# Kernel tuning notes

Measured on AMD Instinct MI355X. Metric: run time of the kernel, lower is better.

Reference implementation:

```python
import jax, jax.numpy as jnp
import numpy as np

NUM_CLASSES = 21  # O + 10 entity types x {B, I}


def setup_inputs() -> dict:
    key = jax.random.key(0)
    k1, k2, k3, k4 = jax.random.split(key, 4)
    S_SENT, L, D = 256, 128, 768
    return {
        "support_emb": jax.random.normal(k1, (S_SENT, L, D), dtype=jnp.float32),
        "query_emb": jax.random.normal(k2, (S_SENT, L, D), dtype=jnp.float32),
        "support_label": jax.random.randint(k3, (S_SENT, L), 0, NUM_CLASSES, dtype=jnp.int32),
        "support_text_mask": jax.random.randint(k4, (S_SENT, L), 0, 2, dtype=jnp.int32),
    }


def reference(support_emb, query_emb, support_label, support_text_mask):
    D = support_emb.shape[-1]
    emb = support_emb.reshape(-1, D)                      # [Ns, D]
    lab = support_label.reshape(-1)                       # [Ns]
    msk = support_text_mask.reshape(-1).astype(emb.dtype) # [Ns]

    # __get_proto__: per-class mean over masked support tokens (segment-mean via one-hot GEMM)
    onehot = jax.nn.one_hot(lab, NUM_CLASSES, dtype=emb.dtype) * msk[:, None]  # [Ns, C]
    class_sum = jnp.einsum("nc,nd->cd", onehot, emb)      # [C, D]
    counts = onehot.sum(axis=0)                           # [C]
    proto = jnp.where(counts[:, None] > 0,
                      class_sum / jnp.maximum(counts, 1.0)[:, None],
                      0.0)                                 # absent classes -> zero vector

    # __batch_dist__: -||q - p||^2 expanded as GEMM (same math, no NxCxD tensor)
    Q = query_emb.reshape(-1, D)                          # [Nq, D] (query mask all-ones)
    logits = (2.0 * Q @ proto.T
              - jnp.sum(Q * Q, axis=-1, keepdims=True)
              - jnp.sum(proto * proto, axis=-1)[None, :])  # [Nq, C]

    pred = jnp.argmax(logits, axis=1)
    return logits, pred
```

## Files before the change

kernel.cpp:

```cpp
#include <hip/hip_runtime.h>

#define NS 32768
#define NQ 32768
#define DIM 768
#define NC 21

#define WS_CS    0
#define WS_CNT   16128
#define WS_PROTO 16384
#define WS_PNORM 32512
#define WS_ZERO_FLOATS 16384

__global__ __launch_bounds__(256) void k_counts(const int* __restrict__ lab,
                                                const int* __restrict__ msk,
                                                float* __restrict__ ws) {
    __shared__ int cnt[NC];
    int tid = threadIdx.x;
    if (tid < NC) cnt[tid] = 0;
    __syncthreads();
    int idx = blockIdx.x * 256 + tid;
    int stride = gridDim.x * 256;
    for (int i = idx; i < NS; i += stride) {
        if (msk[i]) atomicAdd(&cnt[lab[i]], 1);
    }
    __syncthreads();
    if (tid < NC && cnt[tid] > 0) atomicAdd(&ws[WS_CNT + tid], (float)cnt[tid]);
}

#define K1_TOK 256
#define K1_DCOLS 256
__global__ __launch_bounds__(256) void k_classsum(const float* __restrict__ emb,
                                                  const int* __restrict__ lab,
                                                  const int* __restrict__ msk,
                                                  float* __restrict__ ws) {
    __shared__ float acc[NC][K1_DCOLS];
    int tid = threadIdx.x;
    for (int i = tid; i < NC * K1_DCOLS; i += 256) ((float*)acc)[i] = 0.f;
    __syncthreads();

    int chunk = blockIdx.x;
    int dblk  = blockIdx.y;
    int dbase = dblk * K1_DCOLS;
    int t0    = chunk * K1_TOK;
    const float* ebase = emb + (size_t)t0 * DIM + dbase;

    #pragma unroll 1
    for (int tt = 0; tt < K1_TOK; tt += 4) {
        float v0 = ebase[(size_t)(tt + 0) * DIM + tid];
        float v1 = ebase[(size_t)(tt + 1) * DIM + tid];
        float v2 = ebase[(size_t)(tt + 2) * DIM + tid];
        float v3 = ebase[(size_t)(tt + 3) * DIM + tid];
        int t = t0 + tt;
        int c0 = lab[t + 0], m0 = msk[t + 0];
        int c1 = lab[t + 1], m1 = msk[t + 1];
        int c2 = lab[t + 2], m2 = msk[t + 2];
        int c3 = lab[t + 3], m3 = msk[t + 3];
        if (m0) acc[c0][tid] += v0;
        if (m1) acc[c1][tid] += v1;
        if (m2) acc[c2][tid] += v2;
        if (m3) acc[c3][tid] += v3;
    }
    __syncthreads();

    #pragma unroll
    for (int c = 0; c < NC; ++c) {
        atomicAdd(&ws[WS_CS + c * DIM + dbase + tid], acc[c][tid]);
    }
}

__global__ __launch_bounds__(256) void k_proto(float* __restrict__ ws) {
    int c = blockIdx.x;
    int tid = threadIdx.x;
    float cnt = ws[WS_CNT + c];
    float scale = (cnt > 0.f) ? (1.f / cnt) : 0.f;
    float ssq = 0.f;
    for (int d = tid; d < DIM; d += 256) {
        float p = ws[WS_CS + c * DIM + d] * scale;
        ws[WS_PROTO + c * DIM + d] = p;
        ssq += p * p;
    }
    #pragma unroll
    for (int m = 32; m; m >>= 1) ssq += __shfl_xor(ssq, m);
    __shared__ float w4[4];
    if ((tid & 63) == 0) w4[tid >> 6] = ssq;
    __syncthreads();
    if (tid == 0) ws[WS_PNORM + c] = w4[0] + w4[1] + w4[2] + w4[3];
}

__global__ __launch_bounds__(256) void k_logits(const float* __restrict__ qemb,
                                                const float* __restrict__ ws,
                                                float* __restrict__ out) {
    int wid  = threadIdx.x >> 6;
    int lane = threadIdx.x & 63;
    int q = blockIdx.x * 4 + wid;

    const float4* q4 = (const float4*)qemb + (size_t)q * (DIM / 4);
    float4 a = q4[lane], b = q4[lane + 64], c4 = q4[lane + 128];

    float qn = a.x * a.x + a.y * a.y + a.z * a.z + a.w * a.w
             + b.x * b.x + b.y * b.y + b.z * b.z + b.w * b.w
             + c4.x * c4.x + c4.y * c4.y + c4.z * c4.z + c4.w * c4.w;
    #pragma unroll
    for (int m = 32; m; m >>= 1) qn += __shfl_xor(qn, m);

    const float4* p4 = (const float4*)(ws + WS_PROTO);
    float logit[NC];
    #pragma unroll
    for (int c = 0; c < NC; ++c) {
        const float4* pr = p4 + c * (DIM / 4);
        float4 x = pr[lane], y = pr[lane + 64], z = pr[lane + 128];
        float d = a.x * x.x + a.y * x.y + a.z * x.z + a.w * x.w
                + b.x * y.x + b.y * y.y + b.z * y.z + b.w * y.w
                + c4.x * z.x + c4.y * z.y + c4.z * z.z + c4.w * z.w;
        #pragma unroll
        for (int m = 32; m; m >>= 1) d += __shfl_xor(d, m);
        logit[c] = 2.f * d - qn - ws[WS_PNORM + c];
    }

    float best = logit[0];
    int bi = 0;
    #pragma unroll
    for (int c = 1; c < NC; ++c) {
        if (logit[c] > best) { best = logit[c]; bi = c; }
    }

    float myv = 0.f;
    #pragma unroll
    for (int c = 0; c < NC; ++c) myv = (lane == c) ? logit[c] : myv;
    float* lrow = out + (size_t)q * NC;
    if (lane < NC) lrow[lane] = myv;
    if (lane == 0) out[(size_t)NQ * NC + q] = (float)bi;
}

extern "C" void kernel_launch(void* const* d_in, const int* in_sizes, int n_in,
                              void* d_out, int out_size, void* d_ws, size_t ws_size,
                              hipStream_t stream) {
    const float* semb = (const float*)d_in[0];
    const float* qemb = (const float*)d_in[1];
    const int*   lab  = (const int*)d_in[2];
    const int*   msk  = (const int*)d_in[3];
    float* ws  = (float*)d_ws;
    float* out = (float*)d_out;

    hipMemsetAsync(d_ws, 0, WS_ZERO_FLOATS * sizeof(float), stream);
    k_counts<<<64, 256, 0, stream>>>(lab, msk, ws);
    k_classsum<<<dim3(NS / K1_TOK, 3), 256, 0, stream>>>(semb, lab, msk, ws);
    k_proto<<<NC, 256, 0, stream>>>(ws);
    k_logits<<<NQ / 4, 256, 0, stream>>>(qemb, ws, out);
}
```

Measured before the change: 305.6 us.

## Fuse proto into logits, register-accumulate class sums, multi-row DPP reductions

Class sums are accumulated in per-thread registers using wave-uniform labels broadcast via readfirstlane and select-FMA, replacing shared-memory read-modify-write, with a one-step prefetch of embedding rows. The separate prototype kernel is removed; each logits block normalizes class sums into shared memory and computes prototype norms itself. The logits kernel processes four query rows per wave with DPP-based wave reductions and defers the query-norm subtraction until after the argmax. This trades redundant per-block prototype setup and more register pressure for fewer launches and less global/LDS traffic.

```diff
diff --git a/kernel.cpp b/kernel.cpp
--- a/kernel.cpp
+++ b/kernel.cpp
@@ -5,11 +5,24 @@
 #define DIM 768
 #define NC 21
 
-#define WS_CS    0
-#define WS_CNT   16128
-#define WS_PROTO 16384
-#define WS_PNORM 32512
-#define WS_ZERO_FLOATS 16384
+#define WS_CS   0
+#define WS_CNT  16128
+#define WS_ZERO 16149
+
+__device__ inline float wave_allsum(float x) {
+    x += __shfl_xor(x, 32);
+    x += __shfl_xor(x, 16);
+    int xi;
+    xi = __builtin_amdgcn_update_dpp(0, __float_as_int(x), 0x128, 0xF, 0xF, false);
+    x += __int_as_float(xi);
+    xi = __builtin_amdgcn_update_dpp(0, __float_as_int(x), 0x124, 0xF, 0xF, false);
+    x += __int_as_float(xi);
+    xi = __builtin_amdgcn_update_dpp(0, __float_as_int(x), 0x122, 0xF, 0xF, false);
+    x += __int_as_float(xi);
+    xi = __builtin_amdgcn_update_dpp(0, __float_as_int(x), 0x121, 0xF, 0xF, false);
+    x += __int_as_float(xi);
+    return x;
+}
 
 __global__ __launch_bounds__(256) void k_counts(const int* __restrict__ lab,
                                                 const int* __restrict__ msk,
@@ -27,109 +40,165 @@
     if (tid < NC && cnt[tid] > 0) atomicAdd(&ws[WS_CNT + tid], (float)cnt[tid]);
 }
 
-#define K1_TOK 256
-#define K1_DCOLS 256
-__global__ __launch_bounds__(256) void k_classsum(const float* __restrict__ emb,
+__global__ __launch_bounds__(768) void k_classsum(const float* __restrict__ emb,
                                                   const int* __restrict__ lab,
                                                   const int* __restrict__ msk,
                                                   float* __restrict__ ws) {
-    __shared__ float acc[NC][K1_DCOLS];
+    __shared__ int lmc[128];
     int tid = threadIdx.x;
-    for (int i = tid; i < NC * K1_DCOLS; i += 256) ((float*)acc)[i] = 0.f;
-    __syncthreads();
-
-    int chunk = blockIdx.x;
-    int dblk  = blockIdx.y;
-    int dbase = dblk * K1_DCOLS;
-    int t0    = chunk * K1_TOK;
-    const float* ebase = emb + (size_t)t0 * DIM + dbase;
-
-    #pragma unroll 1
-    for (int tt = 0; tt < K1_TOK; tt += 4) {
-        float v0 = ebase[(size_t)(tt + 0) * DIM + tid];
-        float v1 = ebase[(size_t)(tt + 1) * DIM + tid];
-        float v2 = ebase[(size_t)(tt + 2) * DIM + tid];
-        float v3 = ebase[(size_t)(tt + 3) * DIM + tid];
-        int t = t0 + tt;
-        int c0 = lab[t + 0], m0 = msk[t + 0];
-        int c1 = lab[t + 1], m1 = msk[t + 1];
-        int c2 = lab[t + 2], m2 = msk[t + 2];
-        int c3 = lab[t + 3], m3 = msk[t + 3];
-        if (m0) acc[c0][tid] += v0;
-        if (m1) acc[c1][tid] += v1;
-        if (m2) acc[c2][tid] += v2;
-        if (m3) acc[c3][tid] += v3;
-    }
-    __syncthreads();
-
-    #pragma unroll
+    int t0 = blockIdx.x * 128;
+    if (tid < 128) {
+        int i = t0 + tid;
+        lmc[tid] = msk[i] ? lab[i] : 255;
+    }
+    __syncthreads();
+
+    float acc[NC];
+#pragma unroll
+    for (int c = 0; c < NC; ++c) acc[c] = 0.f;
+
+    const float* ecol = emb + (size_t)t0 * DIM + tid;
+
+    auto process = [&](int tb, float v0, float v1, float v2, float v3) {
+        int cu0 = __builtin_amdgcn_readfirstlane(lmc[tb + 0]);
+        int cu1 = __builtin_amdgcn_readfirstlane(lmc[tb + 1]);
+        int cu2 = __builtin_amdgcn_readfirstlane(lmc[tb + 2]);
+        int cu3 = __builtin_amdgcn_readfirstlane(lmc[tb + 3]);
+#pragma unroll
+        for (int c = 0; c < NC; ++c) {
+            float s0 = (cu0 == c) ? 1.f : 0.f;
+            float s1 = (cu1 == c) ? 1.f : 0.f;
+            float s2 = (cu2 == c) ? 1.f : 0.f;
+            float s3 = (cu3 == c) ? 1.f : 0.f;
+            acc[c] = fmaf(s0, v0, acc[c]);
+            acc[c] = fmaf(s1, v1, acc[c]);
+            acc[c] = fmaf(s2, v2, acc[c]);
+            acc[c] = fmaf(s3, v3, acc[c]);
+        }
+    };
+
+    float v0 = ecol[(size_t)0 * DIM];
+    float v1 = ecol[(size_t)1 * DIM];
+    float v2 = ecol[(size_t)2 * DIM];
+    float v3 = ecol[(size_t)3 * DIM];
+    for (int g = 0; g < 31; ++g) {
+        int tb = g * 4;
+        float n0 = ecol[(size_t)(tb + 4) * DIM];
+        float n1 = ecol[(size_t)(tb + 5) * DIM];
+        float n2 = ecol[(size_t)(tb + 6) * DIM];
+        float n3 = ecol[(size_t)(tb + 7) * DIM];
+        process(tb, v0, v1, v2, v3);
+        v0 = n0; v1 = n1; v2 = n2; v3 = n3;
+    }
+    process(124, v0, v1, v2, v3);
+
+#pragma unroll
     for (int c = 0; c < NC; ++c) {
-        atomicAdd(&ws[WS_CS + c * DIM + dbase + tid], acc[c][tid]);
-    }
-}
-
-__global__ __launch_bounds__(256) void k_proto(float* __restrict__ ws) {
-    int c = blockIdx.x;
+        atomicAdd(&ws[WS_CS + c * DIM + tid], acc[c]);
+    }
+}
+
+#define LB 64
+__global__ __launch_bounds__(256, 2) void k_logits(const float* __restrict__ qemb,
+                                                   const float* __restrict__ ws,
+                                                   float* __restrict__ out) {
+    __shared__ __align__(16) float pshared[NC * DIM];
+    __shared__ float pnorm[NC];
+    __shared__ float crecip[NC + 3];
     int tid = threadIdx.x;
-    float cnt = ws[WS_CNT + c];
-    float scale = (cnt > 0.f) ? (1.f / cnt) : 0.f;
-    float ssq = 0.f;
-    for (int d = tid; d < DIM; d += 256) {
-        float p = ws[WS_CS + c * DIM + d] * scale;
-        ws[WS_PROTO + c * DIM + d] = p;
-        ssq += p * p;
-    }
-    #pragma unroll
-    for (int m = 32; m; m >>= 1) ssq += __shfl_xor(ssq, m);
-    __shared__ float w4[4];
-    if ((tid & 63) == 0) w4[tid >> 6] = ssq;
-    __syncthreads();
-    if (tid == 0) ws[WS_PNORM + c] = w4[0] + w4[1] + w4[2] + w4[3];
-}
-
-__global__ __launch_bounds__(256) void k_logits(const float* __restrict__ qemb,
-                                                const float* __restrict__ ws,
-                                                float* __restrict__ out) {
-    int wid  = threadIdx.x >> 6;
-    int lane = threadIdx.x & 63;
-    int q = blockIdx.x * 4 + wid;
-
-    const float4* q4 = (const float4*)qemb + (size_t)q * (DIM / 4);
-    float4 a = q4[lane], b = q4[lane + 64], c4 = q4[lane + 128];
-
-    float qn = a.x * a.x + a.y * a.y + a.z * a.z + a.w * a.w
-             + b.x * b.x + b.y * b.y + b.z * b.z + b.w * b.w
-             + c4.x * c4.x + c4.y * c4.y + c4.z * c4.z + c4.w * c4.w;
-    #pragma unroll
-    for (int m = 32; m; m >>= 1) qn += __shfl_xor(qn, m);
-
-    const float4* p4 = (const float4*)(ws + WS_PROTO);
-    float logit[NC];
-    #pragma unroll
-    for (int c = 0; c < NC; ++c) {
-        const float4* pr = p4 + c * (DIM / 4);
-        float4 x = pr[lane], y = pr[lane + 64], z = pr[lane + 128];
-        float d = a.x * x.x + a.y * x.y + a.z * x.z + a.w * x.w
-                + b.x * y.x + b.y * y.y + b.z * y.z + b.w * y.w
-                + c4.x * z.x + c4.y * z.y + c4.z * z.z + c4.w * z.w;
-        #pragma unroll
-        for (int m = 32; m; m >>= 1) d += __shfl_xor(d, m);
-        logit[c] = 2.f * d - qn - ws[WS_PNORM + c];
-    }
-
-    float best = logit[0];
-    int bi = 0;
-    #pragma unroll
-    for (int c = 1; c < NC; ++c) {
-        if (logit[c] > best) { best = logit[c]; bi = c; }
-    }
-
-    float myv = 0.f;
-    #pragma unroll
-    for (int c = 0; c < NC; ++c) myv = (lane == c) ? logit[c] : myv;
-    float* lrow = out + (size_t)q * NC;
-    if (lane < NC) lrow[lane] = myv;
-    if (lane == 0) out[(size_t)NQ * NC + q] = (float)bi;
+
+    if (tid < NC) {
+        float cv = ws[WS_CNT + tid];
+        crecip[tid] = (cv > 0.f) ? (1.f / cv) : 0.f;
+    }
+    __syncthreads();
+
+    {
+        const float4* cs4 = (const float4*)(ws + WS_CS);
+        float4* ps4 = (float4*)pshared;
+#pragma unroll
+        for (int k = 0; k < 16; ++k) {
+            int i4 = tid + k * 256;
+            if (i4 < NC * DIM / 4) {
+                float4 v = cs4[i4];
+                float r = crecip[i4 / 192];
+                v.x *= r; v.y *= r; v.z *= r; v.w *= r;
+                ps4[i4] = v;
+            }
+        }
+    }
+    __syncthreads();
+
+    int wid = tid >> 6, lane = tid & 63;
+
+    for (int c = wid; c < NC; c += 4) {
+        const float4* pr = (const float4*)(pshared + c * DIM);
+        float s = 0.f;
+#pragma unroll
+        for (int j = 0; j < 3; ++j) {
+            float4 p = pr[lane * 3 + j];
+            s += p.x * p.x + p.y * p.y + p.z * p.z + p.w * p.w;
+        }
+        s = wave_allsum(s);
+        if (lane == 0) pnorm[c] = s;
+    }
+    __syncthreads();
+
+    const float4* q4 = (const float4*)qemb;
+    int rbase = blockIdx.x * LB + wid * 16;
+
+    for (int it = 0; it < 4; ++it) {
+        int r0 = rbase + it * 4;
+
+        float4 q[4][3];
+#pragma unroll
+        for (int r = 0; r < 4; ++r) {
+#pragma unroll
+            for (int s = 0; s < 3; ++s) {
+                q[r][s] = q4[(size_t)(r0 + r) * (DIM / 4) + s * 64 + lane];
+            }
+        }
+
+        float qn[4];
+#pragma unroll
+        for (int r = 0; r < 4; ++r) {
+            float t = 0.f;
+#pragma unroll
+            for (int s = 0; s < 3; ++s) {
+                float4 a = q[r][s];
+                t += a.x * a.x + a.y * a.y + a.z * a.z + a.w * a.w;
+            }
+            qn[r] = wave_allsum(t);
+        }
+
+        float myv[4], best[4];
+        int bi[4];
+#pragma unroll
+        for (int r = 0; r < 4; ++r) { myv[r] = 0.f; best[r] = -3.4e38f; bi[r] = 0; }
+
+#pragma unroll
+        for (int c = 0; c < NC; ++c) {
+            const float4* pr = (const float4*)(pshared + c * DIM);
+            float4 p0 = pr[lane], p1 = pr[lane + 64], p2 = pr[lane + 128];
+            float pn = pnorm[c];
+#pragma unroll
+            for (int r = 0; r < 4; ++r) {
+                float d = q[r][0].x * p0.x + q[r][0].y * p0.y + q[r][0].z * p0.z + q[r][0].w * p0.w
+                        + q[r][1].x * p1.x + q[r][1].y * p1.y + q[r][1].z * p1.z + q[r][1].w * p1.w
+                        + q[r][2].x * p2.x + q[r][2].y * p2.y + q[r][2].z * p2.z + q[r][2].w * p2.w;
+                d = wave_allsum(d);
+                float lc = 2.f * d - pn;
+                myv[r] = (lane == c) ? lc : myv[r];
+                if (lc > best[r]) { best[r] = lc; bi[r] = c; }
+            }
+        }
+
+#pragma unroll
+        for (int r = 0; r < 4; ++r) {
+            if (lane < NC) out[(size_t)(r0 + r) * NC + lane] = myv[r] - qn[r];
+            if (lane == 0) out[(size_t)NQ * NC + (r0 + r)] = (float)bi[r];
+        }
+    }
 }
 
 extern "C" void kernel_launch(void* const* d_in, const int* in_sizes, int n_in,
@@ -142,9 +211,8 @@
     float* ws  = (float*)d_ws;
     float* out = (float*)d_out;
 
-    hipMemsetAsync(d_ws, 0, WS_ZERO_FLOATS * sizeof(float), stream);
+    hipMemsetAsync(d_ws, 0, WS_ZERO * sizeof(float), stream);
     k_counts<<<64, 256, 0, stream>>>(lab, msk, ws);
-    k_classsum<<<dim3(NS / K1_TOK, 3), 256, 0, stream>>>(semb, lab, msk, ws);
-    k_proto<<<NC, 256, 0, stream>>>(ws);
-    k_logits<<<NQ / 4, 256, 0, stream>>>(qemb, ws, out);
-}
+    k_classsum<<<256, 768, 0, stream>>>(semb, lab, msk, ws);
+    k_logits<<<NQ / LB, 256, 0, stream>>>(qemb, ws, out);
+}
```

New measurement: 529.0 us. 73.1% more time.
